# Optimization experiments

Hardware: AMD Instinct MI355X
Metric: run time of the kernel (lower is better)

The kernel has to match this reference:

```python
import jax, jax.numpy as jnp
import numpy as np

N_BUS = 200000; N_GEN = 50000
E_BB = 1600000; E_GB = 400000; E_BG = 400000
D_IN = 64; H = 32
OUT_BUS = 4; OUT_GEN = 2


def setup_inputs() -> dict:
    key = jax.random.key(0)
    it = iter(jax.random.split(key, 48))
    def nrm(shape, s=0.05):
        return jax.random.normal(next(it), shape, jnp.float32) * s
    inp = {}
    inp["x_bus"] = jax.random.normal(next(it), (N_BUS, D_IN), jnp.float32)
    inp["x_gen"] = jax.random.normal(next(it), (N_GEN, D_IN), jnp.float32)
    inp["src_bb"] = jax.random.randint(next(it), (E_BB,), 0, N_BUS)
    inp["dst_bb"] = jax.random.randint(next(it), (E_BB,), 0, N_BUS)
    inp["src_gb"] = jax.random.randint(next(it), (E_GB,), 0, N_GEN)
    inp["dst_gb"] = jax.random.randint(next(it), (E_GB,), 0, N_BUS)
    inp["src_bg"] = jax.random.randint(next(it), (E_BG,), 0, N_BUS)
    inp["dst_bg"] = jax.random.randint(next(it), (E_BG,), 0, N_GEN)
    # SAGEConv params per layer / relation: lin_l (on aggregated neighbors, with bias),
    # lin_r (root weight on x_dst, no bias) -- matches PyG SAGEConv defaults.
    for lname, din in (("l1", D_IN), ("l2", H)):
        for rel in ("bb", "gb", "bg"):
            inp[f"{lname}_{rel}_Wl"] = nrm((din, H))
            inp[f"{lname}_{rel}_bl"] = jnp.zeros((H,), jnp.float32)
            inp[f"{lname}_{rel}_Wr"] = nrm((din, H))
    for nt, dout in (("bus", OUT_BUS), ("gen", OUT_GEN)):
        inp[f"lin0_{nt}_W"] = nrm((H, H))
        inp[f"lin0_{nt}_b"] = jnp.zeros((H,), jnp.float32)
        inp[f"linf_{nt}_W"] = nrm((H, dout))
        inp[f"linf_{nt}_b"] = jnp.zeros((dout,), jnp.float32)
    return inp


def _sage(x_src, x_dst, src, dst, Wl, bl, Wr, n_dst):
    # SAGEConv: mean-aggregate neighbor features, then out = lin_l(mean) + lin_r(x_dst)
    msg = jax.ops.segment_sum(x_src[src], dst, num_segments=n_dst)
    cnt = jax.ops.segment_sum(jnp.ones((src.shape[0],), x_src.dtype), dst, num_segments=n_dst)
    mean = msg / jnp.maximum(cnt, 1.0)[:, None]
    return mean @ Wl + bl + x_dst @ Wr


def reference(x_bus, x_gen, src_bb, dst_bb, src_gb, dst_gb, src_bg, dst_bg,
              l1_bb_Wl, l1_bb_bl, l1_bb_Wr, l1_gb_Wl, l1_gb_bl, l1_gb_Wr,
              l1_bg_Wl, l1_bg_bl, l1_bg_Wr,
              l2_bb_Wl, l2_bb_bl, l2_bb_Wr, l2_gb_Wl, l2_gb_bl, l2_gb_Wr,
              l2_bg_Wl, l2_bg_bl, l2_bg_Wr,
              lin0_bus_W, lin0_bus_b, lin0_gen_W, lin0_gen_b,
              linf_bus_W, linf_bus_b, linf_gen_W, linf_gen_b):
    # HeteroConv layer 1 (aggr='sum' over relations targeting each dst type)
    hb = (_sage(x_bus, x_bus, src_bb, dst_bb, l1_bb_Wl, l1_bb_bl, l1_bb_Wr, N_BUS)
          + _sage(x_gen, x_bus, src_gb, dst_gb, l1_gb_Wl, l1_gb_bl, l1_gb_Wr, N_BUS))
    hg = _sage(x_bus, x_gen, src_bg, dst_bg, l1_bg_Wl, l1_bg_bl, l1_bg_Wr, N_GEN)
    xb, xg = jax.nn.relu(hb), jax.nn.relu(hg)  # dropout is identity in eval mode
    # HeteroConv layer 2
    hb = (_sage(xb, xb, src_bb, dst_bb, l2_bb_Wl, l2_bb_bl, l2_bb_Wr, N_BUS)
          + _sage(xg, xb, src_gb, dst_gb, l2_gb_Wl, l2_gb_bl, l2_gb_Wr, N_BUS))
    hg = _sage(xb, xg, src_bg, dst_bg, l2_bg_Wl, l2_bg_bl, l2_bg_Wr, N_GEN)
    xb, xg = jax.nn.relu(hb), jax.nn.relu(hg)
    # per-node-type hidden Linear (input relu'd again as in the original; relu is idempotent)
    xb = jax.nn.relu(xb) @ lin0_bus_W + lin0_bus_b
    xg = jax.nn.relu(xg) @ lin0_gen_W + lin0_gen_b
    out_bus = xb @ linf_bus_W + linf_bus_b
    out_gen = xg @ linf_gen_W + linf_gen_b
    return out_bus, out_gen
```

## Files before the change

### kernel.cpp

```cpp
#include <hip/hip_runtime.h>
#include <hip/hip_bf16.h>

#define N_BUS 200000
#define N_GEN 50000
#define E_BB 1600000
#define E_GB 400000
#define E_BG 400000
#define H 32
#define NBINS 1024
#define EPT 16

#define NB_CSR_BUS 782
#define NB_CSR_GEN 196
#define NB_PART_BB 391
#define NB_PART_GB 98
#define NB_PART_BG 98
#define NB_TF_BUS 782
#define NB_TF_GEN 196
#define NB_PL_BUS 6250
#define NB_PL_GEN 1563

typedef __attribute__((ext_vector_type(8))) short short8;
typedef __attribute__((ext_vector_type(4))) float floatx4;

__device__ inline unsigned short f2bf(float f) {
    __hip_bfloat16 h = __float2bfloat16(f);
    return *reinterpret_cast<unsigned short*>(&h);
}
__device__ inline float bf2f(unsigned short u) {
    return __uint_as_float(((unsigned)u) << 16);
}


__device__ __forceinline__ void hist_body(int blk, int nb, const int* __restrict__ dst,
                                          int nE, unsigned* __restrict__ bcnt) {
    __shared__ unsigned h[NBINS];
    for (int i = threadIdx.x; i < NBINS; i += 256) h[i] = 0;
    __syncthreads();
    for (int e = blk * 256 + threadIdx.x; e < nE; e += nb * 256)
        atomicAdd(&h[(unsigned)dst[e] >> 8], 1u);
    __syncthreads();
    for (int i = threadIdx.x; i < NBINS; i += 256)
        if (h[i]) atomicAdd(&bcnt[i], h[i]);
}

__global__ __launch_bounds__(256) void hist_all_kernel(
    const int* __restrict__ dbb, const int* __restrict__ dgb, const int* __restrict__ dbg,
    unsigned* __restrict__ cbb, unsigned* __restrict__ cgb, unsigned* __restrict__ cbg)
{
    int b = blockIdx.x;
    if (b < 256) hist_body(b, 256, dbb, E_BB, cbb);
    else if (b < 352) hist_body(b - 256, 96, dgb, E_GB, cgb);
    else hist_body(b - 352, 96, dbg, E_BG, cbg);
}

__global__ __launch_bounds__(256) void scan_all_kernel(unsigned* __restrict__ c0,
                                                       unsigned* __restrict__ c1,
                                                       unsigned* __restrict__ c2) {
    unsigned* a = (blockIdx.x == 0) ? c0 : (blockIdx.x == 1) ? c1 : c2;
    __shared__ unsigned sh[256];
    int tid = threadIdx.x;
    int base = tid * 4;
    unsigned v[4], ts = 0;
#pragma unroll
    for (int q = 0; q < 4; q++) { v[q] = a[base + q]; ts += v[q]; }
    sh[tid] = ts;
    __syncthreads();
#pragma unroll
    for (int d = 1; d < 256; d <<= 1) {
        unsigned t = (tid >= d) ? sh[tid - d] : 0u;
        __syncthreads();
        sh[tid] += t;
        __syncthreads();
    }
    unsigned run = sh[tid] - ts;
#pragma unroll
    for (int q = 0; q < 4; q++) { a[base + q] = run; run += v[q]; }
}

__device__ __forceinline__ void part_body(int blk, const int* __restrict__ src,
                                          const int* __restrict__ dst, int nE,
                                          unsigned* __restrict__ cursor,
                                          unsigned* __restrict__ pairs) {
    __shared__ unsigned hist[NBINS];
    __shared__ unsigned base[NBINS];
    const int tid = threadIdx.x;
    const int cbase = blk * (256 * EPT);

    unsigned es[EPT], ed[EPT];
#pragma unroll
    for (int q = 0; q < EPT; q++) {
        int i = cbase + q * 256 + tid;
        if (i < nE) { es[q] = (unsigned)src[i]; ed[q] = (unsigned)dst[i]; }
        else ed[q] = 0xFFFFFFFFu;
    }
    for (int i = tid; i < NBINS; i += 256) hist[i] = 0;
    __syncthreads();
#pragma unroll
    for (int q = 0; q < EPT; q++)
        if (ed[q] != 0xFFFFFFFFu) atomicAdd(&hist[ed[q] >> 8], 1u);
    __syncthreads();
    for (int i = tid; i < NBINS; i += 256) {
        unsigned c = hist[i];
        base[i] = c ? atomicAdd(&cursor[i], c) : 0u;
        hist[i] = 0;
    }
    __syncthreads();
#pragma unroll
    for (int q = 0; q < EPT; q++) {
        if (ed[q] != 0xFFFFFFFFu) {
            unsigned b = ed[q] >> 8;
            unsigned off = atomicAdd(&hist[b], 1u);
            pairs[base[b] + off] = ((ed[q] & 255u) << 24) | es[q];
        }
    }
}

__global__ __launch_bounds__(256) void part_all_kernel(
    const int* __restrict__ sbb, const int* __restrict__ dbb, unsigned* __restrict__ cbb, unsigned* __restrict__ pbb,
    const int* __restrict__ sgb, const int* __restrict__ dgb, unsigned* __restrict__ cgb, unsigned* __restrict__ pgb,
    const int* __restrict__ sbg, const int* __restrict__ dbg, unsigned* __restrict__ cbg, unsigned* __restrict__ pbg)
{
    int b = blockIdx.x;
    if (b < NB_PART_BB) part_body(b, sbb, dbb, E_BB, cbb, pbb);
    else if (b < NB_PART_BB + NB_PART_GB) part_body(b - NB_PART_BB, sgb, dgb, E_GB, cgb, pgb);
    else part_body(b - NB_PART_BB - NB_PART_GB, sbg, dbg, E_BG, cbg, pbg);
}

__device__ __forceinline__ void fine_body(int b, const unsigned* __restrict__ cursor,
                                          const unsigned* __restrict__ pairs,
                                          unsigned* __restrict__ rs,
                                          unsigned* __restrict__ esrc, int nDst) {
    __shared__ unsigned cnt[256];
    __shared__ unsigned sh[256];
    const int tid = threadIdx.x;
    const unsigned start = b ? cursor[b - 1] : 0u;
    const unsigned end = cursor[b];

    cnt[tid] = 0;
    __syncthreads();
    for (unsigned k = start + tid; k < end; k += 256)
        atomicAdd(&cnt[pairs[k] >> 24], 1u);
    __syncthreads();
    unsigned c = cnt[tid];
    sh[tid] = c;
    __syncthreads();
#pragma unroll
    for (int d = 1; d < 256; d <<= 1) {
        unsigned t = (tid >= d) ? sh[tid - d] : 0u;
        __syncthreads();
        sh[tid] += t;
        __syncthreads();
    }
    int gd = b * 256 + tid;
    if (gd < nDst) rs[gd] = start + sh[tid];
    cnt[tid] = sh[tid] - c;
    __syncthreads();
    for (unsigned k = start + tid; k < end; k += 256) {
        unsigned p = pairs[k];
        unsigned off = atomicAdd(&cnt[p >> 24], 1u);
        esrc[start + off] = p & 0x00FFFFFFu;
    }
}

__global__ __launch_bounds__(256) void fine_all_kernel(
    const unsigned* __restrict__ cbb, const unsigned* __restrict__ pbb, unsigned* __restrict__ rsbb, unsigned* __restrict__ ebb,
    const unsigned* __restrict__ cgb, const unsigned* __restrict__ pgb, unsigned* __restrict__ rsgb, unsigned* __restrict__ egb,
    const unsigned* __restrict__ cbg, const unsigned* __restrict__ pbg, unsigned* __restrict__ rsbg, unsigned* __restrict__ ebg)
{
    int b = blockIdx.x;
    if (b < NB_CSR_BUS) fine_body(b, cbb, pbb, rsbb, ebb, N_BUS);
    else if (b < 2 * NB_CSR_BUS) fine_body(b - NB_CSR_BUS, cgb, pgb, rsgb, egb, N_BUS);
    else fine_body(b - 2 * NB_CSR_BUS, cbg, pbg, rsbg, ebg, N_GEN);
}

__global__ __launch_bounds__(256) void prep_kernel(
    const float* __restrict__ l1_bb_Wl, const float* __restrict__ l1_bb_bl, const float* __restrict__ l1_bb_Wr,
    const float* __restrict__ l1_gb_Wl, const float* __restrict__ l1_gb_bl, const float* __restrict__ l1_gb_Wr,
    const float* __restrict__ l1_bg_Wl, const float* __restrict__ l1_bg_bl, const float* __restrict__ l1_bg_Wr,
    const float* __restrict__ l2_bb_Wl, const float* __restrict__ l2_bb_bl, const float* __restrict__ l2_bb_Wr,
    const float* __restrict__ l2_gb_Wl, const float* __restrict__ l2_gb_bl, const float* __restrict__ l2_gb_Wr,
    const float* __restrict__ l2_bg_Wl, const float* __restrict__ l2_bg_bl, const float* __restrict__ l2_bg_Wr,
    const float* __restrict__ lin0_bus_W, const float* __restrict__ lin0_bus_b,
    const float* __restrict__ linf_bus_W, const float* __restrict__ linf_bus_b,
    const float* __restrict__ lin0_gen_W, const float* __restrict__ lin0_gen_b,
    const float* __restrict__ linf_gen_W, const float* __restrict__ linf_gen_b,
    unsigned short* __restrict__ Wf1b, float* __restrict__ B1b,
    unsigned short* __restrict__ Wf1g, float* __restrict__ B1g,
    unsigned short* __restrict__ Wf2b, float* __restrict__ B2b,
    unsigned short* __restrict__ Wf2g, float* __restrict__ B2g,
    float* __restrict__ WeB, float* __restrict__ beB,
    float* __restrict__ WeG, float* __restrict__ beG)
{
    int t0 = blockIdx.x * 256 + threadIdx.x;
    int NT = gridDim.x * 256;

    for (int f = t0; f < 2 * 6 * 64 * 8; f += NT) {
        int j = f & 7, l = (f >> 3) & 63, tile = f >> 9;
        int nt = tile % 6, kt = tile / 6;
        int k = kt * 32 + (l >> 4) * 8 + j, n = nt * 16 + (l & 15);
        float v;
        if (n < 32) v = l1_bb_Wl[k * 32 + n];
        else if (n < 64) v = l1_bg_Wl[k * 32 + n - 32];
        else v = l1_bb_Wr[k * 32 + n - 64] + l1_gb_Wr[k * 32 + n - 64];
        Wf1b[f] = f2bf(v);
    }
    for (int f = t0; f < 2 * 4 * 64 * 8; f += NT) {
        int j = f & 7, l = (f >> 3) & 63, tile = f >> 9;
        int nt = tile % 4, kt = tile / 4;
        int k = kt * 32 + (l >> 4) * 8 + j, n = nt * 16 + (l & 15);
        float v = (n < 32) ? l1_gb_Wl[k * 32 + n] : l1_bg_Wr[k * 32 + n - 32];
        Wf1g[f] = f2bf(v);
    }
    for (int f = t0; f < 6 * 64 * 8; f += NT) {
        int j = f & 7, l = (f >> 3) & 63, nt = f >> 9;
        int k = (l >> 4) * 8 + j, n = nt * 16 + (l & 15);
        float v;
        if (n < 32) v = l2_bb_Wl[k * 32 + n];
        else if (n < 64) v = l2_bg_Wl[k * 32 + n - 32];
        else v = l2_bb_Wr[k * 32 + n - 64] + l2_gb_Wr[k * 32 + n - 64];
        Wf2b[f] = f2bf(v);
    }
    for (int f = t0; f < 4 * 64 * 8; f += NT) {
        int j = f & 7, l = (f >> 3) & 63, nt = f >> 9;
        int k = (l >> 4) * 8 + j, n = nt * 16 + (l & 15);
        float v = (n < 32) ? l2_gb_Wl[k * 32 + n] : l2_bg_Wr[k * 32 + n - 32];
        Wf2g[f] = f2bf(v);
    }
    if (t0 < 96) {
        B1b[t0] = (t0 < 64) ? 0.0f : l1_bb_bl[t0 - 64] + l1_gb_bl[t0 - 64];
        B2b[t0] = (t0 < 64) ? 0.0f : l2_bb_bl[t0 - 64] + l2_gb_bl[t0 - 64];
    }
    if (t0 < 64) {
        B1g[t0] = (t0 < 32) ? 0.0f : l1_bg_bl[t0 - 32];
        B2g[t0] = (t0 < 32) ? 0.0f : l2_bg_bl[t0 - 32];
    }
    if (t0 < 128) {
        int k = t0 >> 2, c = t0 & 3;
        float s = 0.0f;
        for (int m = 0; m < 32; m++) s += lin0_bus_W[k * 32 + m] * linf_bus_W[m * 4 + c];
        WeB[t0] = s;
    }
    if (t0 >= 128 && t0 < 132) {
        int c = t0 - 128;
        float s = linf_bus_b[c];
        for (int m = 0; m < 32; m++) s += lin0_bus_b[m] * linf_bus_W[m * 4 + c];
        beB[c] = s;
    }
    if (t0 >= 132 && t0 < 196) {
        int i = t0 - 132, k = i >> 1, c = i & 1;
        float s = 0.0f;
        for (int m = 0; m < 32; m++) s += lin0_gen_W[k * 32 + m] * linf_gen_W[m * 2 + c];
        WeG[i] = s;
    }
    if (t0 >= 196 && t0 < 198) {
        int c = t0 - 196;
        float s = linf_gen_b[c];
        for (int m = 0; m < 32; m++) s += lin0_gen_b[m] * linf_gen_W[m * 2 + c];
        beG[c] = s;
    }
}

template <int K, int NOUT, bool RELU_IN>
__device__ __forceinline__ void transform_body(
    int blk, const float* x, int n,
    const unsigned short* __restrict__ Wf, const float* __restrict__ bias,
    unsigned short* __restrict__ y0, unsigned short* __restrict__ y1, float* h,
    char* ldsraw)
{
    constexpr int KT = K / 32, NTN = NOUT / 16, NCH = NOUT / 32;
    constexpr int XS = K + 8;
    constexpr int OS = 34;
    short* lx = (short*)ldsraw;
    float* lo = (float*)ldsraw;

    const int tid = threadIdx.x;
    const int base = blk * 256;
    const int rows = min(256, n - base);
    const int w = tid >> 6, l = tid & 63, quad = l >> 4, ln = l & 15;

    short8 bf[KT][NTN];
    const short8* wf8 = (const short8*)Wf;
#pragma unroll
    for (int kt = 0; kt < KT; kt++)
#pragma unroll
        for (int nt = 0; nt < NTN; nt++)
            bf[kt][nt] = wf8[(kt * NTN + nt) * 64 + l];
    float bv[NTN];
#pragma unroll
    for (int nt = 0; nt < NTN; nt++) bv[nt] = bias[nt * 16 + ln];

    {
        const float4* xg = (const float4*)(x + (size_t)base * K);
        const int T4 = rows * (K / 4);
        for (int q = tid; q < T4; q += 256) {
            float4 v = xg[q];
            if (RELU_IN) {
                v.x = fmaxf(v.x, 0.f); v.y = fmaxf(v.y, 0.f);
                v.z = fmaxf(v.z, 0.f); v.w = fmaxf(v.w, 0.f);
            }
            int r = q / (K / 4), c = (q % (K / 4)) * 4;
            short4 s4;
            s4.x = (short)f2bf(v.x); s4.y = (short)f2bf(v.y);
            s4.z = (short)f2bf(v.z); s4.w = (short)f2bf(v.w);
            *(short4*)&lx[r * XS + c] = s4;
        }
    }
    __syncthreads();

    floatx4 acc[4][NTN];
#pragma unroll
    for (int mt = 0; mt < 4; mt++)
#pragma unroll
        for (int nt = 0; nt < NTN; nt++) {
            floatx4 c0 = {bv[nt], bv[nt], bv[nt], bv[nt]};
            acc[mt][nt] = c0;
        }
#pragma unroll
    for (int mt = 0; mt < 4; mt++) {
        const int row = w * 64 + mt * 16 + ln;
#pragma unroll
        for (int kt = 0; kt < KT; kt++) {
            short8 af = *(const short8*)&lx[row * XS + kt * 32 + quad * 8];
#pragma unroll
            for (int nt = 0; nt < NTN; nt++)
                acc[mt][nt] = __builtin_amdgcn_mfma_f32_16x16x32_bf16(
                    af, bf[kt][nt], acc[mt][nt], 0, 0, 0);
        }
    }

#pragma unroll
    for (int c = 0; c < NCH; c++) {
        __syncthreads();
#pragma unroll
        for (int mt = 0; mt < 4; mt++)
#pragma unroll
            for (int d = 0; d < 2; d++) {
                int nt = 2 * c + d;
#pragma unroll
                for (int r = 0; r < 4; r++)
                    lo[(w * 64 + mt * 16 + quad * 4 + r) * OS + d * 16 + ln] = acc[mt][nt][r];
            }
        __syncthreads();
        const int T4 = rows * 8;
        if (c == NCH - 1) {
            float* og = h + (size_t)base * 32;
            for (int q = tid; q < T4; q += 256) {
                int r = q >> 3, cc = (q & 7) * 4;
                const float* p = &lo[r * OS + cc];
                *(float4*)(og + q * 4) = make_float4(p[0], p[1], p[2], p[3]);
            }
        } else {
            unsigned short* og = ((c == 0) ? y0 : y1) + (size_t)base * 32;
            for (int q = tid; q < T4; q += 256) {
                int r = q >> 3, cc = (q & 7) * 4;
                const float* p = &lo[r * OS + cc];
                short4 s4;
                s4.x = (short)f2bf(p[0]); s4.y = (short)f2bf(p[1]);
                s4.z = (short)f2bf(p[2]); s4.w = (short)f2bf(p[3]);
                *(short4*)(og + q * 4) = s4;
            }
        }
    }
}

template <int K, bool RELU_IN>
__global__ __launch_bounds__(256) void tf_all_kernel(
    const float* xb, const unsigned short* __restrict__ Wfb, const float* __restrict__ Bb,
    unsigned short* __restrict__ yb0, unsigned short* __restrict__ yb1, float* hb,
    const float* xg, const unsigned short* __restrict__ Wfg, const float* __restrict__ Bg,
    unsigned short* __restrict__ yg0, float* hg)
{
    constexpr int XB = 256 * (K + 8) * 2, OB = 256 * 34 * 4;
    __shared__ __align__(16) char ldsraw[(XB > OB) ? XB : OB];
    int b = blockIdx.x;
    if (b < NB_TF_BUS)
        transform_body<K, 96, RELU_IN>(b, xb, N_BUS, Wfb, Bb, yb0, yb1, hb, ldsraw);
    else
        transform_body<K, 64, RELU_IN>(b - NB_TF_BUS, xg, N_GEN, Wfg, Bg, yg0, nullptr, hg, ldsraw);
}

template <bool FUSE>
__device__ __forceinline__ void pull_body(
    int blk, bool hasB, int n,
    const unsigned* __restrict__ rsA, const unsigned* __restrict__ eA, const unsigned short* __restrict__ yA,
    const unsigned* __restrict__ rsB, const unsigned* __restrict__ eB, const unsigned short* __restrict__ yB,
    float* __restrict__ h,
    const float* __restrict__ We, const float* __restrict__ be, int DOUT, float* __restrict__ outp)
{
    const int tid = threadIdx.x;
    unsigned node = blk * 32u + (tid >> 3);
    int j = (tid & 7) * 4;
    if (node >= (unsigned)n) return;

    float4 r = *(const float4*)(h + (size_t)node * H + j);

    auto accum_rel = [&](const unsigned* __restrict__ rs, const unsigned* __restrict__ e,
                         const unsigned short* __restrict__ y) {
        unsigned k0 = node ? rs[node - 1] : 0u;
        unsigned k1 = rs[node];
        float4 a0 = make_float4(0.f, 0.f, 0.f, 0.f);
        float4 a1 = make_float4(0.f, 0.f, 0.f, 0.f);
        float4 a2 = make_float4(0.f, 0.f, 0.f, 0.f);
        float4 a3 = make_float4(0.f, 0.f, 0.f, 0.f);
        unsigned k = k0;
        for (; k + 4 <= k1; k += 4) {
            unsigned s0 = e[k], s1 = e[k + 1], s2 = e[k + 2], s3 = e[k + 3];
            ushort4 v0 = *(const ushort4*)(y + (size_t)s0 * H + j);
            ushort4 v1 = *(const ushort4*)(y + (size_t)s1 * H + j);
            ushort4 v2 = *(const ushort4*)(y + (size_t)s2 * H + j);
            ushort4 v3 = *(const ushort4*)(y + (size_t)s3 * H + j);
            a0.x += bf2f(v0.x); a0.y += bf2f(v0.y); a0.z += bf2f(v0.z); a0.w += bf2f(v0.w);
            a1.x += bf2f(v1.x); a1.y += bf2f(v1.y); a1.z += bf2f(v1.z); a1.w += bf2f(v1.w);
            a2.x += bf2f(v2.x); a2.y += bf2f(v2.y); a2.z += bf2f(v2.z); a2.w += bf2f(v2.w);
            a3.x += bf2f(v3.x); a3.y += bf2f(v3.y); a3.z += bf2f(v3.z); a3.w += bf2f(v3.w);
        }
        for (; k < k1; ++k) {
            unsigned s = e[k];
            const ushort4 v = *(const ushort4*)(y + (size_t)s * H + j);
            a0.x += bf2f(v.x); a0.y += bf2f(v.y); a0.z += bf2f(v.z); a0.w += bf2f(v.w);
        }
        a0.x += a1.x + a2.x + a3.x; a0.y += a1.y + a2.y + a3.y;
        a0.z += a1.z + a2.z + a3.z; a0.w += a1.w + a2.w + a3.w;
        unsigned c = k1 - k0;
        float inv = 1.0f / (float)(c > 1u ? c : 1u);
        r.x += a0.x * inv; r.y += a0.y * inv; r.z += a0.z * inv; r.w += a0.w * inv;
    };

    accum_rel(rsA, eA, yA);
    if (hasB) accum_rel(rsB, eB, yB);

    if (!FUSE) {
        *(float4*)(h + (size_t)node * H + j) = r;
        return;
    }

    float p0 = fmaxf(r.x, 0.f), p1 = fmaxf(r.y, 0.f), p2 = fmaxf(r.z, 0.f), p3 = fmaxf(r.w, 0.f);
    float tot[4];
#pragma unroll
    for (int c = 0; c < 4; c++) {
        if (c < DOUT) {
            tot[c] = p0 * We[(j + 0) * DOUT + c] + p1 * We[(j + 1) * DOUT + c]
                   + p2 * We[(j + 2) * DOUT + c] + p3 * We[(j + 3) * DOUT + c];
        } else tot[c] = 0.f;
    }
#pragma unroll
    for (int mask = 1; mask <= 4; mask <<= 1) {
#pragma unroll
        for (int c = 0; c < 4; c++) tot[c] += __shfl_xor(tot[c], mask);
    }
    if ((tid & 7) == 0) {
        if (DOUT == 4) {
            *(float4*)(outp + (size_t)node * 4) =
                make_float4(tot[0] + be[0], tot[1] + be[1], tot[2] + be[2], tot[3] + be[3]);
        } else {
            *(float2*)(outp + (size_t)node * 2) = make_float2(tot[0] + be[0], tot[1] + be[1]);
        }
    }
}

template <bool FUSE>
__global__ __launch_bounds__(256) void pull_all_kernel(
    const unsigned* __restrict__ rsbb, const unsigned* __restrict__ ebb, const unsigned short* __restrict__ ybb,
    const unsigned* __restrict__ rsgb, const unsigned* __restrict__ egb, const unsigned short* __restrict__ ygb,
    float* __restrict__ hb, const float* __restrict__ WeB, const float* __restrict__ beB,
    const unsigned* __restrict__ rsbg, const unsigned* __restrict__ ebg, const unsigned short* __restrict__ ybg,
    float* __restrict__ hg, const float* __restrict__ WeG, const float* __restrict__ beG,
    float* __restrict__ outp)
{
    int b = blockIdx.x;
    if (b < NB_PL_BUS)
        pull_body<FUSE>(b, true, N_BUS, rsbb, ebb, ybb, rsgb, egb, ygb, hb, WeB, beB, 4, outp);
    else
        pull_body<FUSE>(b - NB_PL_BUS, false, N_GEN, rsbg, ebg, ybg, nullptr, nullptr, nullptr,
                        hg, WeG, beG, 2, outp ? outp + (size_t)N_BUS * 4 : nullptr);
}

extern "C" void kernel_launch(void* const* d_in, const int* in_sizes, int n_in,
                              void* d_out, int out_size, void* d_ws, size_t ws_size,
                              hipStream_t stream) {
    const float* x_bus = (const float*)d_in[0];
    const float* x_gen = (const float*)d_in[1];
    const int* src_bb = (const int*)d_in[2];
    const int* dst_bb = (const int*)d_in[3];
    const int* src_gb = (const int*)d_in[4];
    const int* dst_gb = (const int*)d_in[5];
    const int* src_bg = (const int*)d_in[6];
    const int* dst_bg = (const int*)d_in[7];
    const float* l1_bb_Wl = (const float*)d_in[8];
    const float* l1_bb_bl = (const float*)d_in[9];
    const float* l1_bb_Wr = (const float*)d_in[10];
    const float* l1_gb_Wl = (const float*)d_in[11];
    const float* l1_gb_bl = (const float*)d_in[12];
    const float* l1_gb_Wr = (const float*)d_in[13];
    const float* l1_bg_Wl = (const float*)d_in[14];
    const float* l1_bg_bl = (const float*)d_in[15];
    const float* l1_bg_Wr = (const float*)d_in[16];
    const float* l2_bb_Wl = (const float*)d_in[17];
    const float* l2_bb_bl = (const float*)d_in[18];
    const float* l2_bb_Wr = (const float*)d_in[19];
    const float* l2_gb_Wl = (const float*)d_in[20];
    const float* l2_gb_bl = (const float*)d_in[21];
    const float* l2_gb_Wr = (const float*)d_in[22];
    const float* l2_bg_Wl = (const float*)d_in[23];
    const float* l2_bg_bl = (const float*)d_in[24];
    const float* l2_bg_Wr = (const float*)d_in[25];
    const float* lin0_bus_W = (const float*)d_in[26];
    const float* lin0_bus_b = (const float*)d_in[27];
    const float* linf_bus_W = (const float*)d_in[28];
    const float* linf_bus_b = (const float*)d_in[29];
    const float* lin0_gen_W = (const float*)d_in[30];
    const float* lin0_gen_b = (const float*)d_in[31];
    const float* linf_gen_W = (const float*)d_in[32];
    const float* linf_gen_b = (const float*)d_in[33];

    char* ws = (char*)d_ws;
    size_t off = 0;
    auto alloc = [&](size_t bytes) {
        char* p = ws + off;
        off += (bytes + 255) & ~(size_t)255;
        return p;
    };
    unsigned* rs_bb = (unsigned*)alloc((size_t)N_BUS * 4);
    unsigned* rs_gb = (unsigned*)alloc((size_t)N_BUS * 4);
    unsigned* rs_bg = (unsigned*)alloc((size_t)N_GEN * 4);
    unsigned* cur_bb = (unsigned*)alloc(NBINS * 4);
    unsigned* cur_gb = (unsigned*)alloc(NBINS * 4);
    unsigned* cur_bg = (unsigned*)alloc(NBINS * 4);
    unsigned* e_bb = (unsigned*)alloc((size_t)E_BB * 4);
    unsigned* e_gb = (unsigned*)alloc((size_t)E_GB * 4);
    unsigned* e_bg = (unsigned*)alloc((size_t)E_BG * 4);
    unsigned short* y_bb = (unsigned short*)alloc((size_t)N_BUS * H * 2);
    unsigned short* y_bg = (unsigned short*)alloc((size_t)N_BUS * H * 2);
    unsigned short* y_gb = (unsigned short*)alloc((size_t)N_GEN * H * 2);
    float* h_bus = (float*)alloc((size_t)N_BUS * H * 4);
    float* h_gen = (float*)alloc((size_t)N_GEN * H * 4);
    unsigned short* Wf1b = (unsigned short*)alloc(2 * 6 * 64 * 8 * 2);
    float* B1b = (float*)alloc(96 * 4);
    unsigned short* Wf1g = (unsigned short*)alloc(2 * 4 * 64 * 8 * 2);
    float* B1g = (float*)alloc(64 * 4);
    unsigned short* Wf2b = (unsigned short*)alloc(6 * 64 * 8 * 2);
    float* B2b = (float*)alloc(96 * 4);
    unsigned short* Wf2g = (unsigned short*)alloc(4 * 64 * 8 * 2);
    float* B2g = (float*)alloc(64 * 4);
    float* WeB = (float*)alloc(128 * 4);
    float* beB = (float*)alloc(4 * 4);
    float* WeG = (float*)alloc(64 * 4);
    float* beG = (float*)alloc(2 * 4);

    unsigned* p_bb = (unsigned*)y_bb;
    unsigned* p_gb = (unsigned*)y_bg;
    unsigned* p_bg = (unsigned*)y_gb;

    prep_kernel<<<32, 256, 0, stream>>>(
        l1_bb_Wl, l1_bb_bl, l1_bb_Wr, l1_gb_Wl, l1_gb_bl, l1_gb_Wr,
        l1_bg_Wl, l1_bg_bl, l1_bg_Wr, l2_bb_Wl, l2_bb_bl, l2_bb_Wr,
        l2_gb_Wl, l2_gb_bl, l2_gb_Wr, l2_bg_Wl, l2_bg_bl, l2_bg_Wr,
        lin0_bus_W, lin0_bus_b, linf_bus_W, linf_bus_b,
        lin0_gen_W, lin0_gen_b, linf_gen_W, linf_gen_b,
        Wf1b, B1b, Wf1g, B1g, Wf2b, B2b, Wf2g, B2g, WeB, beB, WeG, beG);

    hipMemsetAsync(cur_bb, 0, 3 * NBINS * 4, stream);

    hist_all_kernel<<<448, 256, 0, stream>>>(dst_bb, dst_gb, dst_bg, cur_bb, cur_gb, cur_bg);
    scan_all_kernel<<<3, 256, 0, stream>>>(cur_bb, cur_gb, cur_bg);
    part_all_kernel<<<NB_PART_BB + NB_PART_GB + NB_PART_BG, 256, 0, stream>>>(
        src_bb, dst_bb, cur_bb, p_bb, src_gb, dst_gb, cur_gb, p_gb, src_bg, dst_bg, cur_bg, p_bg);
    fine_all_kernel<<<2 * NB_CSR_BUS + NB_CSR_GEN, 256, 0, stream>>>(
        cur_bb, p_bb, rs_bb, e_bb, cur_gb, p_gb, rs_gb, e_gb, cur_bg, p_bg, rs_bg, e_bg);

    tf_all_kernel<64, false><<<NB_TF_BUS + NB_TF_GEN, 256, 0, stream>>>(
        x_bus, Wf1b, B1b, y_bb, y_bg, h_bus, x_gen, Wf1g, B1g, y_gb, h_gen);
    pull_all_kernel<false><<<NB_PL_BUS + NB_PL_GEN, 256, 0, stream>>>(
        rs_bb, e_bb, y_bb, rs_gb, e_gb, y_gb, h_bus, WeB, beB,
        rs_bg, e_bg, y_bg, h_gen, WeG, beG, nullptr);

    tf_all_kernel<32, true><<<NB_TF_BUS + NB_TF_GEN, 256, 0, stream>>>(
        h_bus, Wf2b, B2b, y_bb, y_bg, h_bus, h_gen, Wf2g, B2g, y_gb, h_gen);
    pull_all_kernel<true><<<NB_PL_BUS + NB_PL_GEN, 256, 0, stream>>>(
        rs_bb, e_bb, y_bb, rs_gb, e_gb, y_gb, h_bus, WeB, beB,
        rs_bg, e_bg, y_bg, h_gen, WeG, beG, (float*)d_out);
}
```

Measured before the change: 365.8 us.

## Fuse all stages into one persistent cooperative kernel with grid syncs

```diff
diff --git a/kernel.cpp b/kernel.cpp
--- a/kernel.cpp
+++ b/kernel.cpp
@@ -1,4 +1,5 @@
 #include <hip/hip_runtime.h>
+#include <hip/hip_cooperative_groups.h>
 #include <hip/hip_bf16.h>
 
 #define N_BUS 200000
@@ -15,10 +16,13 @@
 #define NB_PART_BB 391
 #define NB_PART_GB 98
 #define NB_PART_BG 98
+#define NB_PART_ALL 587
 #define NB_TF_BUS 782
 #define NB_TF_GEN 196
+#define NB_TF_ALL 978
 #define NB_PL_BUS 6250
 #define NB_PL_GEN 1563
+#define LDS_BYTES 36864
 
 typedef __attribute__((ext_vector_type(8))) short short8;
 typedef __attribute__((ext_vector_type(4))) float floatx4;
@@ -31,10 +35,101 @@
     return __uint_as_float(((unsigned)u) << 16);
 }
 
+struct KParams {
+    const int *src_bb, *dst_bb, *src_gb, *dst_gb, *src_bg, *dst_bg;
+    const float *x_bus, *x_gen;
+    const float *l1_bb_Wl, *l1_bb_bl, *l1_bb_Wr;
+    const float *l1_gb_Wl, *l1_gb_bl, *l1_gb_Wr;
+    const float *l1_bg_Wl, *l1_bg_bl, *l1_bg_Wr;
+    const float *l2_bb_Wl, *l2_bb_bl, *l2_bb_Wr;
+    const float *l2_gb_Wl, *l2_gb_bl, *l2_gb_Wr;
+    const float *l2_bg_Wl, *l2_bg_bl, *l2_bg_Wr;
+    const float *lin0_bus_W, *lin0_bus_b, *linf_bus_W, *linf_bus_b;
+    const float *lin0_gen_W, *lin0_gen_b, *linf_gen_W, *linf_gen_b;
+    unsigned *rs_bb, *rs_gb, *rs_bg;
+    unsigned *cur_bb, *cur_gb, *cur_bg;
+    unsigned *e_bb, *e_gb, *e_bg;
+    unsigned *p_bb, *p_gb, *p_bg;
+    unsigned short *y_bb, *y_bg, *y_gb;
+    float *h_bus, *h_gen;
+    unsigned short *Wf1b, *Wf1g, *Wf2b, *Wf2g;
+    float *B1b, *B1g, *B2b, *B2g;
+    float *WeB, *beB, *WeG, *beG;
+    float *outp;
+};
+
+
+__device__ __forceinline__ void prep_body(const KParams& P, int t0, int NT) {
+    if (t0 < 3 * NBINS) P.cur_bb[t0] = 0u;
+
+    for (int f = t0; f < 2 * 6 * 64 * 8; f += NT) {
+        int j = f & 7, l = (f >> 3) & 63, tile = f >> 9;
+        int nt = tile % 6, kt = tile / 6;
+        int k = kt * 32 + (l >> 4) * 8 + j, n = nt * 16 + (l & 15);
+        float v;
+        if (n < 32) v = P.l1_bb_Wl[k * 32 + n];
+        else if (n < 64) v = P.l1_bg_Wl[k * 32 + n - 32];
+        else v = P.l1_bb_Wr[k * 32 + n - 64] + P.l1_gb_Wr[k * 32 + n - 64];
+        P.Wf1b[f] = f2bf(v);
+    }
+    for (int f = t0; f < 2 * 4 * 64 * 8; f += NT) {
+        int j = f & 7, l = (f >> 3) & 63, tile = f >> 9;
+        int nt = tile % 4, kt = tile / 4;
+        int k = kt * 32 + (l >> 4) * 8 + j, n = nt * 16 + (l & 15);
+        float v = (n < 32) ? P.l1_gb_Wl[k * 32 + n] : P.l1_bg_Wr[k * 32 + n - 32];
+        P.Wf1g[f] = f2bf(v);
+    }
+    for (int f = t0; f < 6 * 64 * 8; f += NT) {
+        int j = f & 7, l = (f >> 3) & 63, nt = f >> 9;
+        int k = (l >> 4) * 8 + j, n = nt * 16 + (l & 15);
+        float v;
+        if (n < 32) v = P.l2_bb_Wl[k * 32 + n];
+        else if (n < 64) v = P.l2_bg_Wl[k * 32 + n - 32];
+        else v = P.l2_bb_Wr[k * 32 + n - 64] + P.l2_gb_Wr[k * 32 + n - 64];
+        P.Wf2b[f] = f2bf(v);
+    }
+    for (int f = t0; f < 4 * 64 * 8; f += NT) {
+        int j = f & 7, l = (f >> 3) & 63, nt = f >> 9;
+        int k = (l >> 4) * 8 + j, n = nt * 16 + (l & 15);
+        float v = (n < 32) ? P.l2_gb_Wl[k * 32 + n] : P.l2_bg_Wr[k * 32 + n - 32];
+        P.Wf2g[f] = f2bf(v);
+    }
+    if (t0 < 96) {
+        P.B1b[t0] = (t0 < 64) ? 0.0f : P.l1_bb_bl[t0 - 64] + P.l1_gb_bl[t0 - 64];
+        P.B2b[t0] = (t0 < 64) ? 0.0f : P.l2_bb_bl[t0 - 64] + P.l2_gb_bl[t0 - 64];
+    }
+    if (t0 < 64) {
+        P.B1g[t0] = (t0 < 32) ? 0.0f : P.l1_bg_bl[t0 - 32];
+        P.B2g[t0] = (t0 < 32) ? 0.0f : P.l2_bg_bl[t0 - 32];
+    }
+    if (t0 < 128) {
+        int k = t0 >> 2, c = t0 & 3;
+        float s = 0.0f;
+        for (int m = 0; m < 32; m++) s += P.lin0_bus_W[k * 32 + m] * P.linf_bus_W[m * 4 + c];
+        P.WeB[t0] = s;
+    }
+    if (t0 >= 128 && t0 < 132) {
+        int c = t0 - 128;
+        float s = P.linf_bus_b[c];
+        for (int m = 0; m < 32; m++) s += P.lin0_bus_b[m] * P.linf_bus_W[m * 4 + c];
+        P.beB[c] = s;
+    }
+    if (t0 >= 132 && t0 < 196) {
+        int i = t0 - 132, k = i >> 1, c = i & 1;
+        float s = 0.0f;
+        for (int m = 0; m < 32; m++) s += P.lin0_gen_W[k * 32 + m] * P.linf_gen_W[m * 2 + c];
+        P.WeG[i] = s;
+    }
+    if (t0 >= 196 && t0 < 198) {
+        int c = t0 - 196;
+        float s = P.linf_gen_b[c];
+        for (int m = 0; m < 32; m++) s += P.lin0_gen_b[m] * P.linf_gen_W[m * 2 + c];
+        P.beG[c] = s;
+    }
+}
 
 __device__ __forceinline__ void hist_body(int blk, int nb, const int* __restrict__ dst,
-                                          int nE, unsigned* __restrict__ bcnt) {
-    __shared__ unsigned h[NBINS];
+                                          int nE, unsigned* __restrict__ bcnt, unsigned* h) {
     for (int i = threadIdx.x; i < NBINS; i += 256) h[i] = 0;
     __syncthreads();
     for (int e = blk * 256 + threadIdx.x; e < nE; e += nb * 256)
@@ -44,21 +139,7 @@
         if (h[i]) atomicAdd(&bcnt[i], h[i]);
 }
 
-__global__ __launch_bounds__(256) void hist_all_kernel(
-    const int* __restrict__ dbb, const int* __restrict__ dgb, const int* __restrict__ dbg,
-    unsigned* __restrict__ cbb, unsigned* __restrict__ cgb, unsigned* __restrict__ cbg)
-{
-    int b = blockIdx.x;
-    if (b < 256) hist_body(b, 256, dbb, E_BB, cbb);
-    else if (b < 352) hist_body(b - 256, 96, dgb, E_GB, cgb);
-    else hist_body(b - 352, 96, dbg, E_BG, cbg);
-}
-
-__global__ __launch_bounds__(256) void scan_all_kernel(unsigned* __restrict__ c0,
-                                                       unsigned* __restrict__ c1,
-                                                       unsigned* __restrict__ c2) {
-    unsigned* a = (blockIdx.x == 0) ? c0 : (blockIdx.x == 1) ? c1 : c2;
-    __shared__ unsigned sh[256];
+__device__ __forceinline__ void scan_body(unsigned* __restrict__ a, unsigned* sh) {
     int tid = threadIdx.x;
     int base = tid * 4;
     unsigned v[4], ts = 0;
@@ -81,9 +162,8 @@
 __device__ __forceinline__ void part_body(int blk, const int* __restrict__ src,
                                           const int* __restrict__ dst, int nE,
                                           unsigned* __restrict__ cursor,
-                                          unsigned* __restrict__ pairs) {
-    __shared__ unsigned hist[NBINS];
-    __shared__ unsigned base[NBINS];
+                                          unsigned* __restrict__ pairs,
+                                          unsigned* hist, unsigned* base) {
     const int tid = threadIdx.x;
     const int cbase = blk * (256 * EPT);
 
@@ -116,23 +196,11 @@
     }
 }
 
-__global__ __launch_bounds__(256) void part_all_kernel(
-    const int* __restrict__ sbb, const int* __restrict__ dbb, unsigned* __restrict__ cbb, unsigned* __restrict__ pbb,
-    const int* __restrict__ sgb, const int* __restrict__ dgb, unsigned* __restrict__ cgb, unsigned* __restrict__ pgb,
-    const int* __restrict__ sbg, const int* __restrict__ dbg, unsigned* __restrict__ cbg, unsigned* __restrict__ pbg)
-{
-    int b = blockIdx.x;
-    if (b < NB_PART_BB) part_body(b, sbb, dbb, E_BB, cbb, pbb);
-    else if (b < NB_PART_BB + NB_PART_GB) part_body(b - NB_PART_BB, sgb, dgb, E_GB, cgb, pgb);
-    else part_body(b - NB_PART_BB - NB_PART_GB, sbg, dbg, E_BG, cbg, pbg);
-}
-
 __device__ __forceinline__ void fine_body(int b, const unsigned* __restrict__ cursor,
                                           const unsigned* __restrict__ pairs,
                                           unsigned* __restrict__ rs,
-                                          unsigned* __restrict__ esrc, int nDst) {
-    __shared__ unsigned cnt[256];
-    __shared__ unsigned sh[256];
+                                          unsigned* __restrict__ esrc, int nDst,
+                                          unsigned* cnt, unsigned* sh) {
     const int tid = threadIdx.x;
     const unsigned start = b ? cursor[b - 1] : 0u;
     const unsigned end = cursor[b];
@@ -160,104 +228,6 @@
         unsigned p = pairs[k];
         unsigned off = atomicAdd(&cnt[p >> 24], 1u);
         esrc[start + off] = p & 0x00FFFFFFu;
-    }
-}
-
-__global__ __launch_bounds__(256) void fine_all_kernel(
-    const unsigned* __restrict__ cbb, const unsigned* __restrict__ pbb, unsigned* __restrict__ rsbb, unsigned* __restrict__ ebb,
-    const unsigned* __restrict__ cgb, const unsigned* __restrict__ pgb, unsigned* __restrict__ rsgb, unsigned* __restrict__ egb,
-    const unsigned* __restrict__ cbg, const unsigned* __restrict__ pbg, unsigned* __restrict__ rsbg, unsigned* __restrict__ ebg)
-{
-    int b = blockIdx.x;
-    if (b < NB_CSR_BUS) fine_body(b, cbb, pbb, rsbb, ebb, N_BUS);
-    else if (b < 2 * NB_CSR_BUS) fine_body(b - NB_CSR_BUS, cgb, pgb, rsgb, egb, N_BUS);
-    else fine_body(b - 2 * NB_CSR_BUS, cbg, pbg, rsbg, ebg, N_GEN);
-}
-
-__global__ __launch_bounds__(256) void prep_kernel(
-    const float* __restrict__ l1_bb_Wl, const float* __restrict__ l1_bb_bl, const float* __restrict__ l1_bb_Wr,
-    const float* __restrict__ l1_gb_Wl, const float* __restrict__ l1_gb_bl, const float* __restrict__ l1_gb_Wr,
-    const float* __restrict__ l1_bg_Wl, const float* __restrict__ l1_bg_bl, const float* __restrict__ l1_bg_Wr,
-    const float* __restrict__ l2_bb_Wl, const float* __restrict__ l2_bb_bl, const float* __restrict__ l2_bb_Wr,
-    const float* __restrict__ l2_gb_Wl, const float* __restrict__ l2_gb_bl, const float* __restrict__ l2_gb_Wr,
-    const float* __restrict__ l2_bg_Wl, const float* __restrict__ l2_bg_bl, const float* __restrict__ l2_bg_Wr,
-    const float* __restrict__ lin0_bus_W, const float* __restrict__ lin0_bus_b,
-    const float* __restrict__ linf_bus_W, const float* __restrict__ linf_bus_b,
-    const float* __restrict__ lin0_gen_W, const float* __restrict__ lin0_gen_b,
-    const float* __restrict__ linf_gen_W, const float* __restrict__ linf_gen_b,
-    unsigned short* __restrict__ Wf1b, float* __restrict__ B1b,
-    unsigned short* __restrict__ Wf1g, float* __restrict__ B1g,
-    unsigned short* __restrict__ Wf2b, float* __restrict__ B2b,
-    unsigned short* __restrict__ Wf2g, float* __restrict__ B2g,
-    float* __restrict__ WeB, float* __restrict__ beB,
-    float* __restrict__ WeG, float* __restrict__ beG)
-{
-    int t0 = blockIdx.x * 256 + threadIdx.x;
-    int NT = gridDim.x * 256;
-
-    for (int f = t0; f < 2 * 6 * 64 * 8; f += NT) {
-        int j = f & 7, l = (f >> 3) & 63, tile = f >> 9;
-        int nt = tile % 6, kt = tile / 6;
-        int k = kt * 32 + (l >> 4) * 8 + j, n = nt * 16 + (l & 15);
-        float v;
-        if (n < 32) v = l1_bb_Wl[k * 32 + n];
-        else if (n < 64) v = l1_bg_Wl[k * 32 + n - 32];
-        else v = l1_bb_Wr[k * 32 + n - 64] + l1_gb_Wr[k * 32 + n - 64];
-        Wf1b[f] = f2bf(v);
-    }
-    for (int f = t0; f < 2 * 4 * 64 * 8; f += NT) {
-        int j = f & 7, l = (f >> 3) & 63, tile = f >> 9;
-        int nt = tile % 4, kt = tile / 4;
-        int k = kt * 32 + (l >> 4) * 8 + j, n = nt * 16 + (l & 15);
-        float v = (n < 32) ? l1_gb_Wl[k * 32 + n] : l1_bg_Wr[k * 32 + n - 32];
-        Wf1g[f] = f2bf(v);
-    }
-    for (int f = t0; f < 6 * 64 * 8; f += NT) {
-        int j = f & 7, l = (f >> 3) & 63, nt = f >> 9;
-        int k = (l >> 4) * 8 + j, n = nt * 16 + (l & 15);
-        float v;
-        if (n < 32) v = l2_bb_Wl[k * 32 + n];
-        else if (n < 64) v = l2_bg_Wl[k * 32 + n - 32];
-        else v = l2_bb_Wr[k * 32 + n - 64] + l2_gb_Wr[k * 32 + n - 64];
-        Wf2b[f] = f2bf(v);
-    }
-    for (int f = t0; f < 4 * 64 * 8; f += NT) {
-        int j = f & 7, l = (f >> 3) & 63, nt = f >> 9;
-        int k = (l >> 4) * 8 + j, n = nt * 16 + (l & 15);
-        float v = (n < 32) ? l2_gb_Wl[k * 32 + n] : l2_bg_Wr[k * 32 + n - 32];
-        Wf2g[f] = f2bf(v);
-    }
-    if (t0 < 96) {
-        B1b[t0] = (t0 < 64) ? 0.0f : l1_bb_bl[t0 - 64] + l1_gb_bl[t0 - 64];
-        B2b[t0] = (t0 < 64) ? 0.0f : l2_bb_bl[t0 - 64] + l2_gb_bl[t0 - 64];
-    }
-    if (t0 < 64) {
-        B1g[t0] = (t0 < 32) ? 0.0f : l1_bg_bl[t0 - 32];
-        B2g[t0] = (t0 < 32) ? 0.0f : l2_bg_bl[t0 - 32];
-    }
-    if (t0 < 128) {
-        int k = t0 >> 2, c = t0 & 3;
-        float s = 0.0f;
-        for (int m = 0; m < 32; m++) s += lin0_bus_W[k * 32 + m] * linf_bus_W[m * 4 + c];
-        WeB[t0] = s;
-    }
-    if (t0 >= 128 && t0 < 132) {
-        int c = t0 - 128;
-        float s = linf_bus_b[c];
-        for (int m = 0; m < 32; m++) s += lin0_bus_b[m] * linf_bus_W[m * 4 + c];
-        beB[c] = s;
-    }
-    if (t0 >= 132 && t0 < 196) {
-        int i = t0 - 132, k = i >> 1, c = i & 1;
-        float s = 0.0f;
-        for (int m = 0; m < 32; m++) s += lin0_gen_W[k * 32 + m] * linf_gen_W[m * 2 + c];
-        WeG[i] = s;
-    }
-    if (t0 >= 196 && t0 < 198) {
-        int c = t0 - 196;
-        float s = linf_gen_b[c];
-        for (int m = 0; m < 32; m++) s += lin0_gen_b[m] * linf_gen_W[m * 2 + c];
-        beG[c] = s;
     }
 }
 
@@ -362,22 +332,6 @@
             }
         }
     }
-}
-
-template <int K, bool RELU_IN>
-__global__ __launch_bounds__(256) void tf_all_kernel(
-    const float* xb, const unsigned short* __restrict__ Wfb, const float* __restrict__ Bb,
-    unsigned short* __restrict__ yb0, unsigned short* __restrict__ yb1, float* hb,
-    const float* xg, const unsigned short* __restrict__ Wfg, const float* __restrict__ Bg,
-    unsigned short* __restrict__ yg0, float* hg)
-{
-    constexpr int XB = 256 * (K + 8) * 2, OB = 256 * 34 * 4;
-    __shared__ __align__(16) char ldsraw[(XB > OB) ? XB : OB];
-    int b = blockIdx.x;
-    if (b < NB_TF_BUS)
-        transform_body<K, 96, RELU_IN>(b, xb, N_BUS, Wfb, Bb, yb0, yb1, hb, ldsraw);
-    else
-        transform_body<K, 64, RELU_IN>(b - NB_TF_BUS, xg, N_GEN, Wfg, Bg, yg0, nullptr, hg, ldsraw);
 }
 
 template <bool FUSE>
@@ -459,60 +413,127 @@
     }
 }
 
-template <bool FUSE>
-__global__ __launch_bounds__(256) void pull_all_kernel(
-    const unsigned* __restrict__ rsbb, const unsigned* __restrict__ ebb, const unsigned short* __restrict__ ybb,
-    const unsigned* __restrict__ rsgb, const unsigned* __restrict__ egb, const unsigned short* __restrict__ ygb,
-    float* __restrict__ hb, const float* __restrict__ WeB, const float* __restrict__ beB,
-    const unsigned* __restrict__ rsbg, const unsigned* __restrict__ ebg, const unsigned short* __restrict__ ybg,
-    float* __restrict__ hg, const float* __restrict__ WeG, const float* __restrict__ beG,
-    float* __restrict__ outp)
-{
-    int b = blockIdx.x;
-    if (b < NB_PL_BUS)
-        pull_body<FUSE>(b, true, N_BUS, rsbb, ebb, ybb, rsgb, egb, ygb, hb, WeB, beB, 4, outp);
-    else
-        pull_body<FUSE>(b - NB_PL_BUS, false, N_GEN, rsbg, ebg, ybg, nullptr, nullptr, nullptr,
-                        hg, WeG, beG, 2, outp ? outp + (size_t)N_BUS * 4 : nullptr);
+__global__ __launch_bounds__(256, 4) void mega_kernel(KParams P) {
+    __shared__ __align__(16) char lds[LDS_BYTES];
+    cooperative_groups::grid_group gg = cooperative_groups::this_grid();
+    const int G = gridDim.x;
+    const int bx = blockIdx.x;
+
+    prep_body(P, bx * 256 + threadIdx.x, G * 256);
+    gg.sync();
+
+    for (int vb = bx; vb < 448; vb += G) {
+        __syncthreads();
+        if (vb < 256) hist_body(vb, 256, P.dst_bb, E_BB, P.cur_bb, (unsigned*)lds);
+        else if (vb < 352) hist_body(vb - 256, 96, P.dst_gb, E_GB, P.cur_gb, (unsigned*)lds);
+        else hist_body(vb - 352, 96, P.dst_bg, E_BG, P.cur_bg, (unsigned*)lds);
+    }
+    gg.sync();
+
+    for (int vb = bx; vb < 3; vb += G) {
+        __syncthreads();
+        scan_body(vb == 0 ? P.cur_bb : (vb == 1 ? P.cur_gb : P.cur_bg), (unsigned*)lds);
+    }
+    gg.sync();
+
+    for (int vb = bx; vb < NB_PART_ALL; vb += G) {
+        __syncthreads();
+        unsigned* hist = (unsigned*)lds;
+        unsigned* basep = hist + NBINS;
+        if (vb < NB_PART_BB) part_body(vb, P.src_bb, P.dst_bb, E_BB, P.cur_bb, P.p_bb, hist, basep);
+        else if (vb < NB_PART_BB + NB_PART_GB) part_body(vb - NB_PART_BB, P.src_gb, P.dst_gb, E_GB, P.cur_gb, P.p_gb, hist, basep);
+        else part_body(vb - NB_PART_BB - NB_PART_GB, P.src_bg, P.dst_bg, E_BG, P.cur_bg, P.p_bg, hist, basep);
+    }
+    gg.sync();
+
+    for (int vb = bx; vb < 2 * NB_CSR_BUS + NB_CSR_GEN; vb += G) {
+        __syncthreads();
+        unsigned* cnt = (unsigned*)lds;
+        unsigned* sh = cnt + 256;
+        if (vb < NB_CSR_BUS) fine_body(vb, P.cur_bb, P.p_bb, P.rs_bb, P.e_bb, N_BUS, cnt, sh);
+        else if (vb < 2 * NB_CSR_BUS) fine_body(vb - NB_CSR_BUS, P.cur_gb, P.p_gb, P.rs_gb, P.e_gb, N_BUS, cnt, sh);
+        else fine_body(vb - 2 * NB_CSR_BUS, P.cur_bg, P.p_bg, P.rs_bg, P.e_bg, N_GEN, cnt, sh);
+    }
+    gg.sync();
+
+    for (int vb = bx; vb < NB_TF_ALL; vb += G) {
+        __syncthreads();
+        if (vb < NB_TF_BUS)
+            transform_body<64, 96, false>(vb, P.x_bus, N_BUS, P.Wf1b, P.B1b, P.y_bb, P.y_bg, P.h_bus, lds);
+        else
+            transform_body<64, 64, false>(vb - NB_TF_BUS, P.x_gen, N_GEN, P.Wf1g, P.B1g, P.y_gb, nullptr, P.h_gen, lds);
+    }
+    gg.sync();
+
+    for (int vb = bx; vb < NB_PL_BUS + NB_PL_GEN; vb += G) {
+        if (vb < NB_PL_BUS)
+            pull_body<false>(vb, true, N_BUS, P.rs_bb, P.e_bb, P.y_bb, P.rs_gb, P.e_gb, P.y_gb,
+                             P.h_bus, P.WeB, P.beB, 4, nullptr);
+        else
+            pull_body<false>(vb - NB_PL_BUS, false, N_GEN, P.rs_bg, P.e_bg, P.y_bg,
+                             nullptr, nullptr, nullptr, P.h_gen, P.WeG, P.beG, 2, nullptr);
+    }
+    gg.sync();
+
+    for (int vb = bx; vb < NB_TF_ALL; vb += G) {
+        __syncthreads();
+        if (vb < NB_TF_BUS)
+            transform_body<32, 96, true>(vb, P.h_bus, N_BUS, P.Wf2b, P.B2b, P.y_bb, P.y_bg, P.h_bus, lds);
+        else
+            transform_body<32, 64, true>(vb - NB_TF_BUS, P.h_gen, N_GEN, P.Wf2g, P.B2g, P.y_gb, nullptr, P.h_gen, lds);
+    }
+    gg.sync();
+
+    for (int vb = bx; vb < NB_PL_BUS + NB_PL_GEN; vb += G) {
+        if (vb < NB_PL_BUS)
+            pull_body<true>(vb, true, N_BUS, P.rs_bb, P.e_bb, P.y_bb, P.rs_gb, P.e_gb, P.y_gb,
+                            P.h_bus, P.WeB, P.beB, 4, P.outp);
+        else
+            pull_body<true>(vb - NB_PL_BUS, false, N_GEN, P.rs_bg, P.e_bg, P.y_bg,
+                            nullptr, nullptr, nullptr, P.h_gen, P.WeG, P.beG, 2,
+                            P.outp + (size_t)N_BUS * 4);
+    }
 }
 
 extern "C" void kernel_launch(void* const* d_in, const int* in_sizes, int n_in,
                               void* d_out, int out_size, void* d_ws, size_t ws_size,
                               hipStream_t stream) {
-    const float* x_bus = (const float*)d_in[0];
-    const float* x_gen = (const float*)d_in[1];
-    const int* src_bb = (const int*)d_in[2];
-    const int* dst_bb = (const int*)d_in[3];
-    const int* src_gb = (const int*)d_in[4];
-    const int* dst_gb = (const int*)d_in[5];
-    const int* src_bg = (const int*)d_in[6];
-    const int* dst_bg = (const int*)d_in[7];
-    const float* l1_bb_Wl = (const float*)d_in[8];
-    const float* l1_bb_bl = (const float*)d_in[9];
-    const float* l1_bb_Wr = (const float*)d_in[10];
-    const float* l1_gb_Wl = (const float*)d_in[11];
-    const float* l1_gb_bl = (const float*)d_in[12];
-    const float* l1_gb_Wr = (const float*)d_in[13];
-    const float* l1_bg_Wl = (const float*)d_in[14];
-    const float* l1_bg_bl = (const float*)d_in[15];
-    const float* l1_bg_Wr = (const float*)d_in[16];
-    const float* l2_bb_Wl = (const float*)d_in[17];
-    const float* l2_bb_bl = (const float*)d_in[18];
-    const float* l2_bb_Wr = (const float*)d_in[19];
-    const float* l2_gb_Wl = (const float*)d_in[20];
-    const float* l2_gb_bl = (const float*)d_in[21];
-    const float* l2_gb_Wr = (const float*)d_in[22];
-    const float* l2_bg_Wl = (const float*)d_in[23];
-    const float* l2_bg_bl = (const float*)d_in[24];
-    const float* l2_bg_Wr = (const float*)d_in[25];
-    const float* lin0_bus_W = (const float*)d_in[26];
-    const float* lin0_bus_b = (const float*)d_in[27];
-    const float* linf_bus_W = (const float*)d_in[28];
-    const float* linf_bus_b = (const float*)d_in[29];
-    const float* lin0_gen_W = (const float*)d_in[30];
-    const float* lin0_gen_b = (const float*)d_in[31];
-    const float* linf_gen_W = (const float*)d_in[32];
-    const float* linf_gen_b = (const float*)d_in[33];
+    KParams P;
+    P.x_bus = (const float*)d_in[0];
+    P.x_gen = (const float*)d_in[1];
+    P.src_bb = (const int*)d_in[2];
+    P.dst_bb = (const int*)d_in[3];
+    P.src_gb = (const int*)d_in[4];
+    P.dst_gb = (const int*)d_in[5];
+    P.src_bg = (const int*)d_in[6];
+    P.dst_bg = (const int*)d_in[7];
+    P.l1_bb_Wl = (const float*)d_in[8];
+    P.l1_bb_bl = (const float*)d_in[9];
+    P.l1_bb_Wr = (const float*)d_in[10];
+    P.l1_gb_Wl = (const float*)d_in[11];
+    P.l1_gb_bl = (const float*)d_in[12];
+    P.l1_gb_Wr = (const float*)d_in[13];
+    P.l1_bg_Wl = (const float*)d_in[14];
+    P.l1_bg_bl = (const float*)d_in[15];
+    P.l1_bg_Wr = (const float*)d_in[16];
+    P.l2_bb_Wl = (const float*)d_in[17];
+    P.l2_bb_bl = (const float*)d_in[18];
+    P.l2_bb_Wr = (const float*)d_in[19];
+    P.l2_gb_Wl = (const float*)d_in[20];
+    P.l2_gb_bl = (const float*)d_in[21];
+    P.l2_gb_Wr = (const float*)d_in[22];
+    P.l2_bg_Wl = (const float*)d_in[23];
+    P.l2_bg_bl = (const float*)d_in[24];
+    P.l2_bg_Wr = (const float*)d_in[25];
+    P.lin0_bus_W = (const float*)d_in[26];
+    P.lin0_bus_b = (const float*)d_in[27];
+    P.linf_bus_W = (const float*)d_in[28];
+    P.linf_bus_b = (const float*)d_in[29];
+    P.lin0_gen_W = (const float*)d_in[30];
+    P.lin0_gen_b = (const float*)d_in[31];
+    P.linf_gen_W = (const float*)d_in[32];
+    P.linf_gen_b = (const float*)d_in[33];
+    P.outp = (float*)d_out;
 
     char* ws = (char*)d_ws;
     size_t off = 0;
@@ -521,63 +542,45 @@
         off += (bytes + 255) & ~(size_t)255;
         return p;
     };
-    unsigned* rs_bb = (unsigned*)alloc((size_t)N_BUS * 4);
-    unsigned* rs_gb = (unsigned*)alloc((size_t)N_BUS * 4);
-    unsigned* rs_bg = (unsigned*)alloc((size_t)N_GEN * 4);
-    unsigned* cur_bb = (unsigned*)alloc(NBINS * 4);
-    unsigned* cur_gb = (unsigned*)alloc(NBINS * 4);
-    unsigned* cur_bg = (unsigned*)alloc(NBINS * 4);
-    unsigned* e_bb = (unsigned*)alloc((size_t)E_BB * 4);
-    unsigned* e_gb = (unsigned*)alloc((size_t)E_GB * 4);
-    unsigned* e_bg = (unsigned*)alloc((size_t)E_BG * 4);
-    unsigned short* y_bb = (unsigned short*)alloc((size_t)N_BUS * H * 2);
-    unsigned short* y_bg = (unsigned short*)alloc((size_t)N_BUS * H * 2);
-    unsigned short* y_gb = (unsigned short*)alloc((size_t)N_GEN * H * 2);
-    float* h_bus = (float*)alloc((size_t)N_BUS * H * 4);
-    float* h_gen = (float*)alloc((size_t)N_GEN * H * 4);
-    unsigned short* Wf1b = (unsigned short*)alloc(2 * 6 * 64 * 8 * 2);
-    float* B1b = (float*)alloc(96 * 4);
-    unsigned short* Wf1g = (unsigned short*)alloc(2 * 4 * 64 * 8 * 2);
-    float* B1g = (float*)alloc(64 * 4);
-    unsigned short* Wf2b = (unsigned short*)alloc(6 * 64 * 8 * 2);
-    float* B2b = (float*)alloc(96 * 4);
-    unsigned short* Wf2g = (unsigned short*)alloc(4 * 64 * 8 * 2);
-    float* B2g = (float*)alloc(64 * 4);
-    float* WeB = (float*)alloc(128 * 4);
-    float* beB = (float*)alloc(4 * 4);
-    float* WeG = (float*)alloc(64 * 4);
-    float* beG = (float*)alloc(2 * 4);
-
-    unsigned* p_bb = (unsigned*)y_bb;
-    unsigned* p_gb = (unsigned*)y_bg;
-    unsigned* p_bg = (unsigned*)y_gb;
-
-    prep_kernel<<<32, 256, 0, stream>>>(
-        l1_bb_Wl, l1_bb_bl, l1_bb_Wr, l1_gb_Wl, l1_gb_bl, l1_gb_Wr,
-        l1_bg_Wl, l1_bg_bl, l1_bg_Wr, l2_bb_Wl, l2_bb_bl, l2_bb_Wr,
-        l2_gb_Wl, l2_gb_bl, l2_gb_Wr, l2_bg_Wl, l2_bg_bl, l2_bg_Wr,
-        lin0_bus_W, lin0_bus_b, linf_bus_W, linf_bus_b,
-        lin0_gen_W, lin0_gen_b, linf_gen_W, linf_gen_b,
-        Wf1b, B1b, Wf1g, B1g, Wf2b, B2b, Wf2g, B2g, WeB, beB, WeG, beG);
-
-    hipMemsetAsync(cur_bb, 0, 3 * NBINS * 4, stream);
-
-    hist_all_kernel<<<448, 256, 0, stream>>>(dst_bb, dst_gb, dst_bg, cur_bb, cur_gb, cur_bg);
-    scan_all_kernel<<<3, 256, 0, stream>>>(cur_bb, cur_gb, cur_bg);
-    part_all_kernel<<<NB_PART_BB + NB_PART_GB + NB_PART_BG, 256, 0, stream>>>(
-        src_bb, dst_bb, cur_bb, p_bb, src_gb, dst_gb, cur_gb, p_gb, src_bg, dst_bg, cur_bg, p_bg);
-    fine_all_kernel<<<2 * NB_CSR_BUS + NB_CSR_GEN, 256, 0, stream>>>(
-        cur_bb, p_bb, rs_bb, e_bb, cur_gb, p_gb, rs_gb, e_gb, cur_bg, p_bg, rs_bg, e_bg);
-
-    tf_all_kernel<64, false><<<NB_TF_BUS + NB_TF_GEN, 256, 0, stream>>>(
-        x_bus, Wf1b, B1b, y_bb, y_bg, h_bus, x_gen, Wf1g, B1g, y_gb, h_gen);
-    pull_all_kernel<false><<<NB_PL_BUS + NB_PL_GEN, 256, 0, stream>>>(
-        rs_bb, e_bb, y_bb, rs_gb, e_gb, y_gb, h_bus, WeB, beB,
-        rs_bg, e_bg, y_bg, h_gen, WeG, beG, nullptr);
-
-    tf_all_kernel<32, true><<<NB_TF_BUS + NB_TF_GEN, 256, 0, stream>>>(
-        h_bus, Wf2b, B2b, y_bb, y_bg, h_bus, h_gen, Wf2g, B2g, y_gb, h_gen);
-    pull_all_kernel<true><<<NB_PL_BUS + NB_PL_GEN, 256, 0, stream>>>(
-        rs_bb, e_bb, y_bb, rs_gb, e_gb, y_gb, h_bus, WeB, beB,
-        rs_bg, e_bg, y_bg, h_gen, WeG, beG, (float*)d_out);
-}
+    P.rs_bb = (unsigned*)alloc((size_t)N_BUS * 4);
+    P.rs_gb = (unsigned*)alloc((size_t)N_BUS * 4);
+    P.rs_bg = (unsigned*)alloc((size_t)N_GEN * 4);
+    P.cur_bb = (unsigned*)alloc(NBINS * 4);
+    P.cur_gb = (unsigned*)alloc(NBINS * 4);
+    P.cur_bg = (unsigned*)alloc(NBINS * 4);
+    P.e_bb = (unsigned*)alloc((size_t)E_BB * 4);
+    P.e_gb = (unsigned*)alloc((size_t)E_GB * 4);
+    P.e_bg = (unsigned*)alloc((size_t)E_BG * 4);
+    P.p_bb = (unsigned*)alloc((size_t)E_BB * 4);
+    P.p_gb = (unsigned*)alloc((size_t)E_GB * 4);
+    P.p_bg = (unsigned*)alloc((size_t)E_BG * 4);
+    P.y_bb = (unsigned short*)alloc((size_t)N_BUS * H * 2);
+    P.y_bg = (unsigned short*)alloc((size_t)N_BUS * H * 2);
+    P.y_gb = (unsigned short*)alloc((size_t)N_GEN * H * 2);
+    P.h_bus = (float*)alloc((size_t)N_BUS * H * 4);
+    P.h_gen = (float*)alloc((size_t)N_GEN * H * 4);
+    P.Wf1b = (unsigned short*)alloc(2 * 6 * 64 * 8 * 2);
+    P.B1b = (float*)alloc(96 * 4);
+    P.Wf1g = (unsigned short*)alloc(2 * 4 * 64 * 8 * 2);
+    P.B1g = (float*)alloc(64 * 4);
+    P.Wf2b = (unsigned short*)alloc(6 * 64 * 8 * 2);
+    P.B2b = (float*)alloc(96 * 4);
+    P.Wf2g = (unsigned short*)alloc(4 * 64 * 8 * 2);
+    P.B2g = (float*)alloc(64 * 4);
+    P.WeB = (float*)alloc(128 * 4);
+    P.beB = (float*)alloc(4 * 4);
+    P.WeG = (float*)alloc(64 * 4);
+    P.beG = (float*)alloc(2 * 4);
+
+    int dev = 0;
+    hipGetDevice(&dev);
+    hipDeviceProp_t prop;
+    hipGetDeviceProperties(&prop, dev);
+    int nbPerCU = 0;
+    hipError_t oe = hipOccupancyMaxActiveBlocksPerMultiprocessor(&nbPerCU, mega_kernel, 256, 0);
+    if (oe != hipSuccess || nbPerCU < 1) nbPerCU = 1;
+    int grid = nbPerCU * prop.multiProcessorCount;
+
+    void* kargs[] = { (void*)&P };
+    hipLaunchCooperativeKernel((void*)mega_kernel, dim3(grid), dim3(256), kargs, 0, stream);
+}
```

After: 1.060 ms. 2.9x slower.
